# Performance work log

Measured on AMD Instinct MI355X. Metric: run time of the kernel, lower is better.

Reference implementation:

```python
import jax, jax.numpy as jnp
import numpy as np

NUM_USERS = 100_000
NUM_ITEMS = 50_000
N = NUM_USERS + NUM_ITEMS
E_DIR = 600_000            # directed user->item interactions
E = 2 * E_DIR              # bidirectional edge list used by LGConv
D = 64                     # embed_dim
F_EDGE = 8                 # edge_mlp_input_dim (edge_attr 7 + edge_weight_init 1)
H_MLP = 32                 # edge_mlp_hidden_dim
NUM_ARTISTS = 20_000
NUM_ALBUMS = 40_000
NUM_LAYERS = 3
AUDIO_SCALE = 0.3
META_SCALE = 0.44


def l2norm(x, eps=1e-12):
    # matches torch F.normalize(p=2, dim=-1)
    n = jnp.linalg.norm(x, axis=-1, keepdims=True)
    return x / jnp.maximum(n, eps)


def setup_inputs() -> dict:
    key = jax.random.key(0)
    ks = jax.random.split(key, 12)
    u = jax.random.randint(ks[0], (E_DIR,), 0, NUM_USERS)
    it = jax.random.randint(ks[1], (E_DIR,), 0, NUM_ITEMS) + NUM_USERS
    # bidirectional edges over the concatenated [user; item] node space
    edge_index = jnp.stack([jnp.concatenate([u, it]), jnp.concatenate([it, u])], axis=0)
    return {
        'user_emb_w': 0.01 * jax.random.normal(ks[2], (NUM_USERS, D), jnp.float32),
        'item_audio_emb': jax.random.normal(ks[3], (NUM_ITEMS, D), jnp.float32),
        'artist_emb_w': jax.random.normal(ks[4], (NUM_ARTISTS, D), jnp.float32) * (6.0 / (NUM_ARTISTS + D)) ** 0.5,
        'album_emb_w': jax.random.normal(ks[5], (NUM_ALBUMS, D), jnp.float32) * (6.0 / (NUM_ALBUMS + D)) ** 0.5,
        'mlp_w1': jax.random.normal(ks[6], (F_EDGE, H_MLP), jnp.float32) * (1.0 / F_EDGE) ** 0.5,
        'mlp_b1': jnp.zeros((H_MLP,), jnp.float32),
        'mlp_w2': jax.random.normal(ks[7], (H_MLP, 1), jnp.float32) * (1.0 / H_MLP) ** 0.5,
        'mlp_b2': jnp.zeros((1,), jnp.float32),
        'edge_features': jax.random.uniform(ks[8], (E, F_EDGE), jnp.float32),
        'edge_index': edge_index,
        'artist_ids': jax.random.randint(ks[9], (NUM_ITEMS,), 0, NUM_ARTISTS),
        'album_ids': jax.random.randint(ks[10], (NUM_ITEMS,), 0, NUM_ALBUMS),
    }


def reference(user_emb_w, item_audio_emb, artist_emb_w, album_emb_w,
              mlp_w1, mlp_b1, mlp_w2, mlp_b2, edge_features,
              edge_index, artist_ids, album_ids):
    # Edge weight MLP: Linear -> ReLU -> Linear -> Sigmoid -> squeeze
    h = jax.nn.relu(edge_features @ mlp_w1 + mlp_b1)
    edge_w = jax.nn.sigmoid(h @ mlp_w2 + mlp_b2)[:, 0]  # [E]

    # Node features
    user = l2norm(user_emb_w)
    meta = artist_emb_w[artist_ids] + album_emb_w[album_ids]
    item = l2norm(item_audio_emb * AUDIO_SCALE + meta * META_SCALE)
    x = jnp.concatenate([user, item], axis=0)  # [N, D]

    row, col = edge_index[0], edge_index[1]

    # gcn_norm (add_self_loops=False): deg over destination column
    deg = jax.ops.segment_sum(edge_w, col, num_segments=N)
    dinv = jnp.where(deg > 0, 1.0 / jnp.sqrt(jnp.where(deg > 0, deg, 1.0)), 0.0)
    norm = dinv[row] * edge_w * dinv[col]  # [E]

    acc = x
    for _ in range(NUM_LAYERS):
        msg = norm[:, None] * x[row]                         # gather [E, D]
        x = jax.ops.segment_sum(msg, col, num_segments=N)    # scatter-add
        acc = acc + x
    x = l2norm(acc / (NUM_LAYERS + 1))

    user_emb = x[:NUM_USERS]
    item_emb = x[NUM_USERS:]
    align_loss = jnp.float32(0.0)
    return user_emb, item_emb, align_loss
```

## Files before the change

kernel.cpp:

```cpp
#include <hip/hip_runtime.h>
#include <math.h>

#define NUM_USERS 100000
#define NUM_ITEMS 50000
#define NN 150000
#define EE 1200000
#define NB 586
#define NNP (NB * 256)
#define G8_BLOCKS 4688

typedef unsigned short ushort_t;
typedef unsigned int uint_t;

__device__ __forceinline__ uint_t pack2(float lo, float hi) {
    uint_t a = __float_as_uint(lo);
    uint_t b = __float_as_uint(hi);
    a = (a + 0x7FFFu + ((a >> 16) & 1u)) >> 16;
    b = (b + 0x7FFFu + ((b >> 16) & 1u)) & 0xFFFF0000u;
    return a | b;
}
__device__ __forceinline__ float lo16(uint_t x) { return __uint_as_float(x << 16); }
__device__ __forceinline__ float hi16(uint_t x) { return __uint_as_float(x & 0xFFFF0000u); }

__global__ void mlp_count_kernel(const float* __restrict__ feats,
                                 const float* __restrict__ w1,
                                 const float* __restrict__ b1,
                                 const float* __restrict__ w2,
                                 const float* __restrict__ b2,
                                 const int* __restrict__ col,
                                 int2* __restrict__ er,
                                 int* __restrict__ counts) {
    __shared__ float sw1[256];
    __shared__ float sb1[32];
    __shared__ float sw2[32];
    __shared__ float sb2;
    int t = threadIdx.x;
    sw1[t] = w1[t];
    if (t < 32) { sb1[t] = b1[t]; sw2[t] = w2[t]; }
    if (t == 0) sb2 = b2[0];
    __syncthreads();
    int e = blockIdx.x * 256 + t;
    if (e >= EE) return;
    int c = col[e];
    const float4* fp = (const float4*)(feats + (size_t)e * 8);
    float4 fa = fp[0], fb = fp[1];
    float f[8] = {fa.x, fa.y, fa.z, fa.w, fb.x, fb.y, fb.z, fb.w};
    float s = sb2;
#pragma unroll
    for (int j = 0; j < 32; ++j) {
        float h = sb1[j];
#pragma unroll
        for (int i = 0; i < 8; ++i) h = fmaf(f[i], sw1[i * 32 + j], h);
        h = fmaxf(h, 0.f);
        s = fmaf(h, sw2[j], s);
    }
    float w = 1.f / (1.f + expf(-s));
    int k = atomicAdd(&counts[c], 1);
    er[e] = make_int2(k, __float_as_int(w));
}

__global__ void scan1_kernel(const int* __restrict__ counts,
                             int* __restrict__ offs,
                             int* __restrict__ partials) {
    int i = blockIdx.x * 256 + threadIdx.x;
    int lane = threadIdx.x & 63;
    int v = counts[i];
    int s = v;
#pragma unroll
    for (int off = 1; off < 64; off <<= 1) {
        int u = __shfl_up(s, off, 64);
        if (lane >= off) s += u;
    }
    __shared__ int wsum[4];
    if (lane == 63) wsum[threadIdx.x >> 6] = s;
    __syncthreads();
    int add = 0;
    for (int w = 0; w < (threadIdx.x >> 6); ++w) add += wsum[w];
    offs[i] = s - v + add;
    if (threadIdx.x == 255) partials[blockIdx.x] = s + add;
}

__global__ void scan23_kernel(int* __restrict__ offs,
                              const int* __restrict__ partials) {
    __shared__ int sp[768];
    __shared__ int wsum[4];
    int t = threadIdx.x;
#pragma unroll
    for (int k = 0; k < 3; ++k) {
        int idx = t + k * 256;
        sp[idx] = (idx < NB) ? partials[idx] : 0;
    }
    __syncthreads();
    int v0 = sp[3 * t], v1 = sp[3 * t + 1], v2 = sp[3 * t + 2];
    int tot = v0 + v1 + v2;
    int lane = t & 63;
    int s = tot;
#pragma unroll
    for (int off = 1; off < 64; off <<= 1) {
        int u = __shfl_up(s, off, 64);
        if (lane >= off) s += u;
    }
    if (lane == 63) wsum[t >> 6] = s;
    __syncthreads();
    int add = 0;
    for (int w = 0; w < (t >> 6); ++w) add += wsum[w];
    int excl = s - tot + add;
    sp[3 * t]     = excl;
    sp[3 * t + 1] = excl + v0;
    sp[3 * t + 2] = excl + v0 + v1;
    __syncthreads();
    int base = sp[blockIdx.x];
    int i = blockIdx.x * 256 + t;
    offs[i] = offs[i] + base;
}

__global__ void fill_kernel(const int2* __restrict__ er,
                            const int* __restrict__ row,
                            const int* __restrict__ col,
                            const int* __restrict__ offs,
                            int2* __restrict__ packed) {
    int e = blockIdx.x * 256 + threadIdx.x;
    if (e >= EE) return;
    int2 p = er[e];
    int slot = offs[col[e]] + p.x;
    packed[slot] = make_int2(row[e], p.y);
}

__device__ __forceinline__ void gather_node8(const ushort_t* __restrict__ zin,
                                             const int2* __restrict__ packed,
                                             int beg, int end, unsigned c,
                                             float4& a0, float4& a1) {
    for (int base = beg; base < end; base += 8) {
        int m = end - base; if (m > 8) m = 8;
        int r = 0; float w = 0.f;
        if ((int)c < m) {
            int2 p = packed[base + (int)c];
            r = p.x; w = __int_as_float(p.y);
        }
        int rj[8]; float wj[8]; uint4 vj[8];
#pragma unroll
        for (int u = 0; u < 8; ++u) {
            int idx = (u < m) ? u : (m - 1);
            rj[u] = __shfl(r, idx, 8);
            wj[u] = __shfl(w, u, 8);
        }
#pragma unroll
        for (int u = 0; u < 8; ++u)
            vj[u] = *(const uint4*)(zin + (size_t)(uint_t)rj[u] * 64u + c * 8u);
#pragma unroll
        for (int u = 0; u < 8; ++u) {
            float ww = wj[u]; uint4 v = vj[u];
            a0.x = fmaf(ww, lo16(v.x), a0.x);
            a0.y = fmaf(ww, hi16(v.x), a0.y);
            a0.z = fmaf(ww, lo16(v.y), a0.z);
            a0.w = fmaf(ww, hi16(v.y), a0.w);
            a1.x = fmaf(ww, lo16(v.z), a1.x);
            a1.y = fmaf(ww, hi16(v.z), a1.y);
            a1.z = fmaf(ww, lo16(v.w), a1.z);
            a1.w = fmaf(ww, hi16(v.w), a1.w);
        }
    }
}

__global__ void dinv_init_kernel(const int2* __restrict__ packed,
                                 const int* __restrict__ offs,
                                 const float* __restrict__ user_w,
                                 const float* __restrict__ audio,
                                 const float* __restrict__ artist_w,
                                 const float* __restrict__ album_w,
                                 const int* __restrict__ artist_ids,
                                 const int* __restrict__ album_ids,
                                 float* __restrict__ dinv,
                                 ushort_t* __restrict__ z0) {
    unsigned t = blockIdx.x * 256u + threadIdx.x;
    unsigned node = t >> 3, c = t & 7u;
    if (node >= NN) return;
    int beg = offs[node], end = offs[node + 1];
    float ds = 0.f;
    for (int k = beg + (int)c; k < end; k += 8) ds += __int_as_float(packed[k].y);
    ds += __shfl_xor(ds, 1, 8);
    ds += __shfl_xor(ds, 2, 8);
    ds += __shfl_xor(ds, 4, 8);
    float d = (ds > 0.f) ? rsqrtf(ds) : 0.f;
    if (c == 0) dinv[node] = d;

    size_t ri = (size_t)node * 64u + c * 8u;
    float v[8];
    if (node < NUM_USERS) {
        float4 x0 = *(const float4*)(user_w + ri);
        float4 x1 = *(const float4*)(user_w + ri + 4);
        v[0]=x0.x; v[1]=x0.y; v[2]=x0.z; v[3]=x0.w;
        v[4]=x1.x; v[5]=x1.y; v[6]=x1.z; v[7]=x1.w;
    } else {
        unsigned j = node - NUM_USERS;
        unsigned aid = (unsigned)artist_ids[j], bid = (unsigned)album_ids[j];
        const float* ap = artist_w + (size_t)aid * 64u + c * 8u;
        const float* bp = album_w  + (size_t)bid * 64u + c * 8u;
        const float* up = audio    + (size_t)j   * 64u + c * 8u;
        float4 A0 = *(const float4*)ap, A1 = *(const float4*)(ap + 4);
        float4 B0 = *(const float4*)bp, B1 = *(const float4*)(bp + 4);
        float4 U0 = *(const float4*)up, U1 = *(const float4*)(up + 4);
        v[0] = fmaf(0.44f, A0.x + B0.x, 0.3f * U0.x);
        v[1] = fmaf(0.44f, A0.y + B0.y, 0.3f * U0.y);
        v[2] = fmaf(0.44f, A0.z + B0.z, 0.3f * U0.z);
        v[3] = fmaf(0.44f, A0.w + B0.w, 0.3f * U0.w);
        v[4] = fmaf(0.44f, A1.x + B1.x, 0.3f * U1.x);
        v[5] = fmaf(0.44f, A1.y + B1.y, 0.3f * U1.y);
        v[6] = fmaf(0.44f, A1.z + B1.z, 0.3f * U1.z);
        v[7] = fmaf(0.44f, A1.w + B1.w, 0.3f * U1.w);
    }
    float s = 0.f;
#pragma unroll
    for (int k = 0; k < 8; ++k) s = fmaf(v[k], v[k], s);
    s += __shfl_xor(s, 1, 8);
    s += __shfl_xor(s, 2, 8);
    s += __shfl_xor(s, 4, 8);
    float rn = rsqrtf(fmaxf(s, 1e-24f));
    float scale = ((d > 0.f) ? d : 1.f) * rn;
    uint4 o;
    o.x = pack2(v[0] * scale, v[1] * scale);
    o.y = pack2(v[2] * scale, v[3] * scale);
    o.z = pack2(v[4] * scale, v[5] * scale);
    o.w = pack2(v[6] * scale, v[7] * scale);
    *(uint4*)(z0 + ri) = o;
}

__global__ void spmm_kernel(const ushort_t* __restrict__ zin,
                            const int2* __restrict__ packed,
                            const int* __restrict__ offs,
                            const float* __restrict__ dinv,
                            ushort_t* __restrict__ zout) {
    unsigned t = blockIdx.x * 256u + threadIdx.x;
    unsigned node = t >> 3, c = t & 7u;
    if (node >= NN) return;
    float4 a0 = make_float4(0,0,0,0), a1 = make_float4(0,0,0,0);
    gather_node8(zin, packed, offs[node], offs[node + 1], c, a0, a1);
    float d = dinv[node], dd = d * d;
    uint4 o;
    o.x = pack2(a0.x * dd, a0.y * dd);
    o.y = pack2(a0.z * dd, a0.w * dd);
    o.z = pack2(a1.x * dd, a1.y * dd);
    o.w = pack2(a1.z * dd, a1.w * dd);
    *(uint4*)(zout + (size_t)node * 64u + c * 8u) = o;
}

__global__ void spmm_final_kernel(const ushort_t* __restrict__ z0,
                                  const ushort_t* __restrict__ z1,
                                  const ushort_t* __restrict__ z2,
                                  const int2* __restrict__ packed,
                                  const int* __restrict__ offs,
                                  const float* __restrict__ dinv,
                                  float* __restrict__ out) {
    unsigned t = blockIdx.x * 256u + threadIdx.x;
    unsigned node = t >> 3, c = t & 7u;
    if (node >= NN) return;
    float4 a0 = make_float4(0,0,0,0), a1 = make_float4(0,0,0,0);
    gather_node8(z2, packed, offs[node], offs[node + 1], c, a0, a1);
    float d = dinv[node], dd = d * d;
    size_t ri = (size_t)node * 64u + c * 8u;
    uint4 p0 = *(const uint4*)(z0 + ri);
    uint4 p1 = *(const uint4*)(z1 + ri);
    uint4 p2 = *(const uint4*)(z2 + ri);
    float v[8];
    v[0] = lo16(p0.x) + lo16(p1.x) + lo16(p2.x) + a0.x * dd;
    v[1] = hi16(p0.x) + hi16(p1.x) + hi16(p2.x) + a0.y * dd;
    v[2] = lo16(p0.y) + lo16(p1.y) + lo16(p2.y) + a0.z * dd;
    v[3] = hi16(p0.y) + hi16(p1.y) + hi16(p2.y) + a0.w * dd;
    v[4] = lo16(p0.z) + lo16(p1.z) + lo16(p2.z) + a1.x * dd;
    v[5] = hi16(p0.z) + hi16(p1.z) + hi16(p2.z) + a1.y * dd;
    v[6] = lo16(p0.w) + lo16(p1.w) + lo16(p2.w) + a1.z * dd;
    v[7] = hi16(p0.w) + hi16(p1.w) + hi16(p2.w) + a1.w * dd;
    float s = 0.f;
#pragma unroll
    for (int k = 0; k < 8; ++k) s = fmaf(v[k], v[k], s);
    s += __shfl_xor(s, 1, 8);
    s += __shfl_xor(s, 2, 8);
    s += __shfl_xor(s, 4, 8);
    float n = fmaxf(sqrtf(s) * 0.25f, 1e-12f);
    float inv = 0.25f / n;
    float4 o0 = make_float4(v[0]*inv, v[1]*inv, v[2]*inv, v[3]*inv);
    float4 o1 = make_float4(v[4]*inv, v[5]*inv, v[6]*inv, v[7]*inv);
    *(float4*)(out + ri)     = o0;
    *(float4*)(out + ri + 4) = o1;
    if (t == 0) out[(size_t)NN * 64u] = 0.f;
}

extern "C" void kernel_launch(void* const* d_in, const int* in_sizes, int n_in,
                              void* d_out, int out_size, void* d_ws, size_t ws_size,
                              hipStream_t stream) {
    const float* user_w     = (const float*)d_in[0];
    const float* audio      = (const float*)d_in[1];
    const float* artist_w   = (const float*)d_in[2];
    const float* album_w    = (const float*)d_in[3];
    const float* w1         = (const float*)d_in[4];
    const float* b1         = (const float*)d_in[5];
    const float* w2         = (const float*)d_in[6];
    const float* b2         = (const float*)d_in[7];
    const float* feats      = (const float*)d_in[8];
    const int*   row        = (const int*)d_in[9];
    const int*   col        = row + EE;
    const int*   artist_ids = (const int*)d_in[10];
    const int*   album_ids  = (const int*)d_in[11];
    float* out = (float*)d_out;

    int*      counts   = (int*)d_ws;
    int*      offs     = counts + NNP;
    int*      partials = offs + NNP + 16;
    int2*     er       = (int2*)(partials + 1024);
    float*    dinv     = (float*)(er + EE);
    int2*     packed   = (int2*)(dinv + NN);
    ushort_t* z0       = (ushort_t*)(packed + EE);
    ushort_t* z1       = z0 + (size_t)NN * 64;
    ushort_t* z2       = z1 + (size_t)NN * 64;

    hipMemsetAsync(counts, 0, NNP * sizeof(int), stream);

    mlp_count_kernel<<<(EE + 255) / 256, 256, 0, stream>>>(feats, w1, b1, w2, b2,
                                                           col, er, counts);
    scan1_kernel<<<NB, 256, 0, stream>>>(counts, offs, partials);
    scan23_kernel<<<NB, 256, 0, stream>>>(offs, partials);
    fill_kernel<<<(EE + 255) / 256, 256, 0, stream>>>(er, row, col, offs, packed);
    dinv_init_kernel<<<G8_BLOCKS, 256, 0, stream>>>(packed, offs,
                                                    user_w, audio, artist_w, album_w,
                                                    artist_ids, album_ids, dinv, z0);
    spmm_kernel<<<G8_BLOCKS, 256, 0, stream>>>(z0, packed, offs, dinv, z1);
    spmm_kernel<<<G8_BLOCKS, 256, 0, stream>>>(z1, packed, offs, dinv, z2);
    spmm_final_kernel<<<G8_BLOCKS, 256, 0, stream>>>(z0, z1, z2, packed, offs,
                                                     dinv, out);
}
```

Measured before the change: 318.3 us.

## Fuse scan and CSR fill into one cooperative kernel with grid syncs

The two scan kernels and the fill kernel are merged into one cooperative kernel of 586 blocks that uses grid.sync() between phases. The fill phase becomes a grid-stride loop, and this removes two kernel launches and their boundaries. It also moves the counts atomicAdd ahead of the MLP math so its latency overlaps the compute, and hoists the dinv load ahead of the gather in the spmm kernels. In exchange it relies on cooperative launch support, pays for grid-wide barriers, and runs the fill with fewer threads per edge.

```diff
diff --git a/kernel.cpp b/kernel.cpp
--- a/kernel.cpp
+++ b/kernel.cpp
@@ -1,5 +1,8 @@
 #include <hip/hip_runtime.h>
+#include <hip/hip_cooperative_groups.h>
 #include <math.h>
+
+namespace cg = cooperative_groups;
 
 #define NUM_USERS 100000
 #define NUM_ITEMS 50000
@@ -42,6 +45,7 @@
     int e = blockIdx.x * 256 + t;
     if (e >= EE) return;
     int c = col[e];
+    int k = atomicAdd(&counts[c], 1);
     const float4* fp = (const float4*)(feats + (size_t)e * 8);
     float4 fa = fp[0], fb = fp[1];
     float f[8] = {fa.x, fa.y, fa.z, fa.w, fb.x, fb.y, fb.z, fb.w};
@@ -55,75 +59,74 @@
         s = fmaf(h, sw2[j], s);
     }
     float w = 1.f / (1.f + expf(-s));
-    int k = atomicAdd(&counts[c], 1);
     er[e] = make_int2(k, __float_as_int(w));
 }
 
-__global__ void scan1_kernel(const int* __restrict__ counts,
-                             int* __restrict__ offs,
-                             int* __restrict__ partials) {
-    int i = blockIdx.x * 256 + threadIdx.x;
-    int lane = threadIdx.x & 63;
-    int v = counts[i];
-    int s = v;
-#pragma unroll
-    for (int off = 1; off < 64; off <<= 1) {
-        int u = __shfl_up(s, off, 64);
-        if (lane >= off) s += u;
-    }
-    __shared__ int wsum[4];
-    if (lane == 63) wsum[threadIdx.x >> 6] = s;
-    __syncthreads();
-    int add = 0;
-    for (int w = 0; w < (threadIdx.x >> 6); ++w) add += wsum[w];
-    offs[i] = s - v + add;
-    if (threadIdx.x == 255) partials[blockIdx.x] = s + add;
-}
-
-__global__ void scan23_kernel(int* __restrict__ offs,
-                              const int* __restrict__ partials) {
+__global__ void scan_fill_kernel(const int* __restrict__ counts,
+                                 int* __restrict__ offs,
+                                 int* __restrict__ partials,
+                                 const int2* __restrict__ er,
+                                 const int* __restrict__ row,
+                                 const int* __restrict__ col,
+                                 int2* __restrict__ packed) {
+    cg::grid_group grid = cg::this_grid();
     __shared__ int sp[768];
     __shared__ int wsum[4];
     int t = threadIdx.x;
-#pragma unroll
-    for (int k = 0; k < 3; ++k) {
-        int idx = t + k * 256;
-        sp[idx] = (idx < NB) ? partials[idx] : 0;
-    }
-    __syncthreads();
-    int v0 = sp[3 * t], v1 = sp[3 * t + 1], v2 = sp[3 * t + 2];
-    int tot = v0 + v1 + v2;
+    int i = blockIdx.x * 256 + t;
     int lane = t & 63;
-    int s = tot;
-#pragma unroll
-    for (int off = 1; off < 64; off <<= 1) {
-        int u = __shfl_up(s, off, 64);
-        if (lane >= off) s += u;
-    }
-    if (lane == 63) wsum[t >> 6] = s;
-    __syncthreads();
-    int add = 0;
-    for (int w = 0; w < (t >> 6); ++w) add += wsum[w];
-    int excl = s - tot + add;
-    sp[3 * t]     = excl;
-    sp[3 * t + 1] = excl + v0;
-    sp[3 * t + 2] = excl + v0 + v1;
-    __syncthreads();
-    int base = sp[blockIdx.x];
-    int i = blockIdx.x * 256 + t;
-    offs[i] = offs[i] + base;
-}
-
-__global__ void fill_kernel(const int2* __restrict__ er,
-                            const int* __restrict__ row,
-                            const int* __restrict__ col,
-                            const int* __restrict__ offs,
-                            int2* __restrict__ packed) {
-    int e = blockIdx.x * 256 + threadIdx.x;
-    if (e >= EE) return;
-    int2 p = er[e];
-    int slot = offs[col[e]] + p.x;
-    packed[slot] = make_int2(row[e], p.y);
+
+    {
+        int v = counts[i];
+        int s = v;
+#pragma unroll
+        for (int off = 1; off < 64; off <<= 1) {
+            int u = __shfl_up(s, off, 64);
+            if (lane >= off) s += u;
+        }
+        if (lane == 63) wsum[t >> 6] = s;
+        __syncthreads();
+        int add = 0;
+        for (int w = 0; w < (t >> 6); ++w) add += wsum[w];
+        offs[i] = s - v + add;
+        if (t == 255) partials[blockIdx.x] = s + add;
+    }
+    grid.sync();
+
+    {
+#pragma unroll
+        for (int k = 0; k < 3; ++k) {
+            int idx = t + k * 256;
+            sp[idx] = (idx < NB) ? partials[idx] : 0;
+        }
+        __syncthreads();
+        int v0 = sp[3 * t], v1 = sp[3 * t + 1], v2 = sp[3 * t + 2];
+        int tot = v0 + v1 + v2;
+        int s = tot;
+#pragma unroll
+        for (int off = 1; off < 64; off <<= 1) {
+            int u = __shfl_up(s, off, 64);
+            if (lane >= off) s += u;
+        }
+        __syncthreads();
+        if (lane == 63) wsum[t >> 6] = s;
+        __syncthreads();
+        int add = 0;
+        for (int w = 0; w < (t >> 6); ++w) add += wsum[w];
+        int excl = s - tot + add;
+        sp[3 * t]     = excl;
+        sp[3 * t + 1] = excl + v0;
+        sp[3 * t + 2] = excl + v0 + v1;
+        __syncthreads();
+        offs[i] = offs[i] + sp[blockIdx.x];
+    }
+    grid.sync();
+
+    for (int e = i; e < EE; e += NNP) {
+        int2 p = er[e];
+        int slot = offs[col[e]] + p.x;
+        packed[slot] = make_int2(row[e], p.y);
+    }
 }
 
 __device__ __forceinline__ void gather_node8(const ushort_t* __restrict__ zin,
@@ -233,9 +236,10 @@
     unsigned t = blockIdx.x * 256u + threadIdx.x;
     unsigned node = t >> 3, c = t & 7u;
     if (node >= NN) return;
+    float d = dinv[node];
     float4 a0 = make_float4(0,0,0,0), a1 = make_float4(0,0,0,0);
     gather_node8(zin, packed, offs[node], offs[node + 1], c, a0, a1);
-    float d = dinv[node], dd = d * d;
+    float dd = d * d;
     uint4 o;
     o.x = pack2(a0.x * dd, a0.y * dd);
     o.y = pack2(a0.z * dd, a0.w * dd);
@@ -254,9 +258,10 @@
     unsigned t = blockIdx.x * 256u + threadIdx.x;
     unsigned node = t >> 3, c = t & 7u;
     if (node >= NN) return;
+    float d = dinv[node];
     float4 a0 = make_float4(0,0,0,0), a1 = make_float4(0,0,0,0);
     gather_node8(z2, packed, offs[node], offs[node + 1], c, a0, a1);
-    float d = dinv[node], dd = d * d;
+    float dd = d * d;
     size_t ri = (size_t)node * 64u + c * 8u;
     uint4 p0 = *(const uint4*)(z0 + ri);
     uint4 p1 = *(const uint4*)(z1 + ri);
@@ -317,9 +322,12 @@
 
     mlp_count_kernel<<<(EE + 255) / 256, 256, 0, stream>>>(feats, w1, b1, w2, b2,
                                                            col, er, counts);
-    scan1_kernel<<<NB, 256, 0, stream>>>(counts, offs, partials);
-    scan23_kernel<<<NB, 256, 0, stream>>>(offs, partials);
-    fill_kernel<<<(EE + 255) / 256, 256, 0, stream>>>(er, row, col, offs, packed);
+    {
+        void* args[] = { (void*)&counts, (void*)&offs, (void*)&partials,
+                         (void*)&er, (void*)&row, (void*)&col, (void*)&packed };
+        hipLaunchCooperativeKernel((const void*)scan_fill_kernel,
+                                   dim3(NB), dim3(256), args, 0, stream);
+    }
     dinv_init_kernel<<<G8_BLOCKS, 256, 0, stream>>>(packed, offs,
                                                     user_w, audio, artist_w, album_w,
                                                     artist_ids, album_ids, dinv, z0);
```

Measured after the change: 451.0 us. +41.7%, slower.
